# Kernel optimization log

Hardware: AMD Instinct MI355X
Metric: run time of the kernel (lower is better)

## Reference

```python
import jax, jax.numpy as jnp
import numpy as np

EPS = 1e-5

def _ln(t, g, b):
    m = t.mean(-1, keepdims=True)
    v = ((t - m) ** 2).mean(-1, keepdims=True)
    return (t - m) * jax.lax.rsqrt(v + EPS) * g + b

def _sr(t, w, b, H, W, sr):
    # t: [B, H*W, C] -> spatial-reduction conv -> [B, (H//sr)*(W//sr), C]
    B, L, C = t.shape
    xi = t.transpose(0, 2, 1).reshape(B, C, H, W)
    y = jax.lax.conv_general_dilated(xi, w, (sr, sr), 'VALID',
                                     dimension_numbers=('NCHW', 'OIHW', 'NCHW'))
    return y.reshape(B, C, -1).transpose(0, 2, 1) + b

def setup_inputs() -> dict:
    key = jax.random.key(0)
    ks = jax.random.split(key, 9)
    C, head, sr, H, W = 128, 2, 2, 64, 64
    B, N = 4, 2 * H * W
    s = 0.02
    return {
        'x': jax.random.normal(ks[0], (B, N, C), jnp.float32),
        'qW': jax.random.normal(ks[1], (C, C), jnp.float32) * s,
        'qb': jnp.zeros((C,), jnp.float32),
        'kvW': jax.random.normal(ks[2], (C, 2 * C), jnp.float32) * s,
        'kvb': jnp.zeros((2 * C,), jnp.float32),
        'projW': jax.random.normal(ks[3], (C, C), jnp.float32) * s,
        'projb': jnp.zeros((C,), jnp.float32),
        'srW': jax.random.normal(ks[4], (C, C, sr, sr), jnp.float32) * s,
        'srb': jnp.zeros((C,), jnp.float32),
        'lnW': jnp.ones((C,), jnp.float32),
        'lnB': jnp.zeros((C,), jnp.float32),
        'H': H, 'W': W, 'fuse': 1,
    }

def reference(x, qW, qb, kvW, kvb, projW, projb, srW, srb, lnW, lnB, H, W, fuse):
    head, sr = 2, 2
    B, N, C = x.shape
    Dh = C // head
    scale = Dh ** -0.5
    q = (x @ qW + qb).reshape(B, N, head, Dh).transpose(0, 2, 1, 3)  # [B,h,N,Dh]
    mask = None
    if fuse and sr > 1:
        half = N // 2
        x_rgb = _ln(_sr(x[:, :half, :], srW, srb, H, W, sr), lnW, lnB)
        x_dte = _ln(_sr(x[:, half:, :], srW, srb, H, W, sr), lnW, lnB)
        xkv = jnp.concatenate([x_rgb, x_dte], axis=1)
        M = N // (sr * sr)
        row = jnp.arange(N)[:, None] < half            # query in rgb half
        col = jnp.arange(M)[None, :] < (M // 2)        # key in rgb half
        mask = row == col                              # True on same-modality blocks -> masked
    elif sr > 1:
        xkv = _ln(_sr(x, srW, srb, H, W, sr), lnW, lnB)
    else:
        xkv = x
    M = xkv.shape[1]
    kv = (xkv @ kvW + kvb).reshape(B, M, 2, head, Dh).transpose(2, 0, 3, 1, 4)
    k, v = kv[0], kv[1]                                # [B,h,M,Dh]
    attn = jnp.einsum('bhnd,bhmd->bhnm', q, k) * scale
    if mask is not None:
        attn = jnp.where(mask[None, None], -jnp.inf, attn)
    attn = jax.nn.softmax(attn, axis=-1)
    out = jnp.einsum('bhnm,bhmd->bhnd', attn, v).transpose(0, 2, 1, 3).reshape(B, N, C)
    return out @ projW + projb
```

## Files before the change

### kernel.cpp

```cpp
#include <hip/hip_runtime.h>
#include <hip/hip_bf16.h>

#define LN_EPS 1e-5f

typedef __attribute__((ext_vector_type(8))) short bf16x8_t;
typedef __attribute__((ext_vector_type(4))) float f32x4_t;
typedef __attribute__((ext_vector_type(4))) unsigned short u16x4_t;

#define MFMA16(a, b, c) __builtin_amdgcn_mfma_f32_16x16x32_bf16(a, b, c, 0, 0, 0)

__device__ inline unsigned short f2bf(float f) {
    union { float f; unsigned int u; } v; v.f = f;
    unsigned int r = v.u + 0x7fffu + ((v.u >> 16) & 1u);
    return (unsigned short)(r >> 16);
}

__device__ inline u16x4_t pk4(float a, float b, float c, float d) {
    union { u16x4_t v; __hip_bfloat162 h[2]; } u;
    u.h[0] = __float22bfloat162_rn(float2{a, b});
    u.h[1] = __float22bfloat162_rn(float2{c, d});
    return u.v;
}

__device__ inline size_t fragidx(int row, int k, int KC) {
    return ((size_t)((row >> 4) * KC + (k >> 5))) * 512 +
           (((k >> 3) & 3) * 16 + (row & 15)) * 8 + (k & 7);
}

__global__ void k_prep_w(const float* __restrict__ qW, const float* __restrict__ kvW,
                         const float* __restrict__ projW, const float* __restrict__ srW,
                         unsigned short* __restrict__ qWs, unsigned short* __restrict__ kvWs,
                         unsigned short* __restrict__ projWs, unsigned short* __restrict__ srWs) {
    int i = blockIdx.x * 256 + threadIdx.x;
    if (i < 16384) {
        int n = i & 127, k = i >> 7;
        qWs[fragidx(n, k, 4)] = f2bf(qW[k * 128 + n]);
    } else if (i < 49152) {
        int j = i - 16384; int n = j & 255, k = j >> 8;
        kvWs[fragidx(n, k, 4)] = f2bf(kvW[k * 256 + n]);
    } else if (i < 65536) {
        int j = i - 49152; int n = j & 127, k = j >> 7;
        projWs[fragidx(n, k, 4)] = f2bf(projW[k * 128 + n]);
    } else {
        int j = i - 65536; int n = j >> 9, rem = j & 511, q = rem >> 7, c = rem & 127;
        srWs[fragidx(n, q * 128 + c, 16)] = f2bf(srW[n * 512 + c * 4 + q]);
    }
}

__global__ void k_prep_x(const float* __restrict__ x, unsigned short* __restrict__ xsw,
                         unsigned short* __restrict__ Psw) {
    int i = blockIdx.x * 256 + threadIdx.x;
    int c4 = i & 31;
    int row = i >> 5;
    float4 v = *(const float4*)(x + (size_t)row * 128 + c4 * 4);
    u16x4_t o = pk4(v.x, v.y, v.z, v.w);
    int ch = c4 * 4;
    *(u16x4_t*)(xsw + fragidx(row, ch, 4)) = o;
    int b = row >> 13, n = row & 8191;
    int hf = n >> 12, rem = n & 4095;
    int y = rem >> 6, xc = rem & 63;
    int oy = y >> 1, ky = y & 1, ox = xc >> 1, kx = xc & 1;
    int q = ky * 2 + kx;
    int pos = b * 2048 + hf * 1024 + oy * 32 + ox;
    *(u16x4_t*)(Psw + fragidx(pos, q * 128 + ch, 16)) = o;
}

__global__ __launch_bounds__(256)
void k_convkv(const unsigned short* __restrict__ Psw, const unsigned short* __restrict__ srWs,
              const float* __restrict__ srb, const float* __restrict__ lnW,
              const float* __restrict__ lnB, const unsigned short* __restrict__ kvWs,
              const float* __restrict__ kvb, unsigned short* __restrict__ ksw,
              unsigned short* __restrict__ vsw) {
    const int t = threadIdx.x, w = t >> 6, lane = t & 63;
    const int col = lane & 15, quad = lane >> 4;
    const int rt_l = w >> 1, hf = w & 1;
    const int RT = blockIdx.x * 2 + rt_l;

    __shared__ unsigned short xkvs[2 * 4 * 512];
    __shared__ float lnred[4][16][2];

    f32x4_t acc[4] = {};
    {
        const unsigned short* xp = Psw + (size_t)RT * 16 * 512 + lane * 8;
        const unsigned short* wp = srWs + (size_t)hf * 4 * 16 * 512 + lane * 8;
        for (int kc = 0; kc < 16; kc++) {
            bf16x8_t xb = *(const bf16x8_t*)(xp + (size_t)kc * 512);
            #pragma unroll
            for (int j = 0; j < 4; j++) {
                bf16x8_t wf = *(const bf16x8_t*)(wp + (size_t)(j * 16 + kc) * 512);
                acc[j] = MFMA16(wf, xb, acc[j]);
            }
        }
    }
    float s = 0.f, ss = 0.f;
    #pragma unroll
    for (int j = 0; j < 4; j++) {
        float4 bs = *(const float4*)(srb + hf * 64 + j * 16 + quad * 4);
        acc[j][0] += bs.x; acc[j][1] += bs.y; acc[j][2] += bs.z; acc[j][3] += bs.w;
        #pragma unroll
        for (int r = 0; r < 4; r++) { float v = acc[j][r]; s += v; ss += v * v; }
    }
    s += __shfl_xor(s, 16, 64);  s += __shfl_xor(s, 32, 64);
    ss += __shfl_xor(ss, 16, 64); ss += __shfl_xor(ss, 32, 64);
    if (lane < 16) { lnred[w][lane][0] = s; lnred[w][lane][1] = ss; }
    __syncthreads();
    float stot = s + lnred[w ^ 1][col][0];
    float sstot = ss + lnred[w ^ 1][col][1];
    float mean = stot * (1.0f / 128.0f);
    float var = sstot * (1.0f / 128.0f) - mean * mean;
    float rs = rsqrtf(var + LN_EPS);
    #pragma unroll
    for (int j = 0; j < 4; j++) {
        int f0 = hf * 64 + j * 16 + quad * 4;
        float4 g = *(const float4*)(lnW + f0);
        float4 be = *(const float4*)(lnB + f0);
        u16x4_t o = pk4((acc[j][0] - mean) * rs * g.x + be.x,
                        (acc[j][1] - mean) * rs * g.y + be.y,
                        (acc[j][2] - mean) * rs * g.z + be.z,
                        (acc[j][3] - mean) * rs * g.w + be.w);
        *(u16x4_t*)(xkvs + ((size_t)(rt_l * 4 + (f0 >> 5))) * 512 +
                    (((f0 >> 3) & 3) * 16 + col) * 8 + (f0 & 7)) = o;
    }
    __syncthreads();
    bf16x8_t xf[2][4];
    #pragma unroll
    for (int rt = 0; rt < 2; rt++)
        #pragma unroll
        for (int kc = 0; kc < 4; kc++)
            xf[rt][kc] = *(const bf16x8_t*)(xkvs + (size_t)(rt * 4 + kc) * 512 + lane * 8);
    #pragma unroll
    for (int i = 0; i < 2; i++) {
        const int nt2 = w * 2 + i;
        f32x4_t aK[2] = {};
        #pragma unroll
        for (int kc = 0; kc < 4; kc++) {
            bf16x8_t wf = *(const bf16x8_t*)(kvWs + (size_t)(nt2 * 4 + kc) * 512 + lane * 8);
            aK[0] = MFMA16(wf, xf[0][kc], aK[0]);
            aK[1] = MFMA16(wf, xf[1][kc], aK[1]);
        }
        float4 bs = *(const float4*)(kvb + nt2 * 16 + quad * 4);
        #pragma unroll
        for (int rt = 0; rt < 2; rt++) {
            int p = (blockIdx.x * 2 + rt) * 16 + col;
            int m = p & 2047, bb = p >> 11;
            int bh = bb * 2 + (nt2 >> 2);
            u16x4_t o = pk4(aK[rt][0] + bs.x, aK[rt][1] + bs.y,
                            aK[rt][2] + bs.z, aK[rt][3] + bs.w);
            *(u16x4_t*)(ksw + ((size_t)(bh * 128 + (m >> 4)) * 2 + ((nt2 >> 1) & 1)) * 512 +
                        (((nt2 & 1) * 2 + (quad >> 1)) * 16 + (m & 15)) * 8 + (quad & 1) * 4) = o;
        }
    }
    #pragma unroll
    for (int i = 0; i < 2; i++) {
        const int nt2 = 8 + w * 2 + i;
        f32x4_t aV[2] = {};
        #pragma unroll
        for (int kc = 0; kc < 4; kc++) {
            bf16x8_t wf = *(const bf16x8_t*)(kvWs + (size_t)(nt2 * 4 + kc) * 512 + lane * 8);
            aV[0] = MFMA16(xf[0][kc], wf, aV[0]);
            aV[1] = MFMA16(xf[1][kc], wf, aV[1]);
        }
        int fv = (nt2 - 8) * 16 + col;
        int h = fv >> 6, dd = fv & 63;
        float bv = kvb[128 + fv];
        #pragma unroll
        for (int rt = 0; rt < 2; rt++) {
            int G = (blockIdx.x * 2 + rt) * 16 + quad * 4;
            int bb = G >> 11, m0 = G & 2047;
            int bh = bb * 2 + h;
            u16x4_t o = pk4(aV[rt][0] + bv, aV[rt][1] + bv,
                            aV[rt][2] + bv, aV[rt][3] + bv);
            *(u16x4_t*)(vsw + ((size_t)((bh * 4 + (dd >> 4)) * 64 + (m0 >> 5))) * 512 +
                        (((m0 >> 3) & 3) * 16 + (dd & 15)) * 8 + (m0 & 7)) = o;
        }
    }
}

__global__ __launch_bounds__(512)
void k_attn_f(const unsigned short* __restrict__ xsw, const unsigned short* __restrict__ qWs,
              const float* __restrict__ qb, const unsigned short* __restrict__ ksw,
              const unsigned short* __restrict__ vsw, const unsigned short* __restrict__ projWs,
              const float* __restrict__ projb, float* __restrict__ out) {
    const int blkx = blockIdx.x, mod = blockIdx.y, b = blockIdx.z;
    const int t = threadIdx.x, w = t >> 6, lane = t & 63;
    const int col = lane & 15, quad = lane >> 4;
    const int qt = w & 3, h = w >> 2;
    const int bh = b * 2 + h;

    __shared__ unsigned short qls[16 * 512];
    __shared__ unsigned short pp[8][16][72];

    {
        const int qtile_g = b * 512 + mod * 256 + blkx * 4 + qt;
        f32x4_t acc[4] = {};
        const unsigned short* xp = xsw + (size_t)qtile_g * 4 * 512 + lane * 8;
        const unsigned short* wp = qWs + (size_t)h * 16 * 512 + lane * 8;
        #pragma unroll
        for (int kc = 0; kc < 4; kc++) {
            bf16x8_t xb = *(const bf16x8_t*)(xp + (size_t)kc * 512);
            #pragma unroll
            for (int j = 0; j < 4; j++) {
                bf16x8_t wf = *(const bf16x8_t*)(wp + (size_t)(j * 4 + kc) * 512);
                acc[j] = MFMA16(wf, xb, acc[j]);
            }
        }
        const float sc = 0.125f * 1.44269504089f;
        #pragma unroll
        for (int j = 0; j < 4; j++) {
            float4 bs = *(const float4*)(qb + h * 64 + j * 16 + quad * 4);
            u16x4_t o = pk4((acc[j][0] + bs.x) * sc, (acc[j][1] + bs.y) * sc,
                            (acc[j][2] + bs.z) * sc, (acc[j][3] + bs.w) * sc);
            *(u16x4_t*)(qls + ((size_t)((h * 4 + qt) * 2 + (j >> 1))) * 512 +
                        (((j & 1) * 2 + (quad >> 1)) * 16 + col) * 8 + (quad & 1) * 4) = o;
        }
    }
    const bf16x8_t qf0 = *(const bf16x8_t*)(qls + (size_t)((h * 4 + qt) * 2 + 0) * 512 + lane * 8);
    const bf16x8_t qf1 = *(const bf16x8_t*)(qls + (size_t)((h * 4 + qt) * 2 + 1) * 512 + lane * 8);

    const unsigned short* kp0 = ksw + ((size_t)(bh * 128 + (1 - mod) * 64) * 2) * 512 + lane * 8;
    const unsigned short* vp0 = vsw + ((size_t)(bh * 4) * 64 + (1 - mod) * 32) * 512 + lane * 8;
    const bf16x8_t ones = { 0x3F80, 0x3F80, 0x3F80, 0x3F80,
                            0x3F80, 0x3F80, 0x3F80, 0x3F80 };
    f32x4_t O[4] = {};
    f32x4_t accl = {};

    for (int kt = 0; kt < 16; kt++) {
        bf16x8_t kf[8], vf[8];
        #pragma unroll
        for (int i = 0; i < 8; i++)
            kf[i] = *(const bf16x8_t*)(kp0 + (size_t)(kt * 8 + i) * 512);
        #pragma unroll
        for (int dt = 0; dt < 4; dt++) {
            vf[dt * 2 + 0] = *(const bf16x8_t*)(vp0 + ((size_t)dt * 64 + kt * 2 + 0) * 512);
            vf[dt * 2 + 1] = *(const bf16x8_t*)(vp0 + ((size_t)dt * 64 + kt * 2 + 1) * 512);
        }
        f32x4_t ST[4];
        #pragma unroll
        for (int nb = 0; nb < 4; nb++) {
            f32x4_t sA = {};
            sA = MFMA16(kf[nb * 2 + 0], qf0, sA);
            sA = MFMA16(kf[nb * 2 + 1], qf1, sA);
            ST[nb] = sA;
        }
        #pragma unroll
        for (int nb = 0; nb < 4; nb++) {
            u16x4_t pk = pk4(exp2f(ST[nb][0]), exp2f(ST[nb][1]),
                             exp2f(ST[nb][2]), exp2f(ST[nb][3]));
            *(u16x4_t*)(&pp[w][col][nb * 16 + quad * 4]) = pk;
        }
        bf16x8_t pb0 = *(const bf16x8_t*)(&pp[w][col][quad * 8]);
        bf16x8_t pb1 = *(const bf16x8_t*)(&pp[w][col][32 + quad * 8]);
        accl = MFMA16(ones, pb0, accl);
        accl = MFMA16(ones, pb1, accl);
        #pragma unroll
        for (int dt = 0; dt < 4; dt++) {
            O[dt] = MFMA16(vf[dt * 2 + 0], pb0, O[dt]);
            O[dt] = MFMA16(vf[dt * 2 + 1], pb1, O[dt]);
        }
    }
    __syncthreads();
    {
        float rl = 1.0f / accl[0];
        #pragma unroll
        for (int dt = 0; dt < 4; dt++) {
            u16x4_t o = pk4(O[dt][0] * rl, O[dt][1] * rl, O[dt][2] * rl, O[dt][3] * rl);
            *(u16x4_t*)(qls + ((size_t)(qt * 4 + h * 2 + (dt >> 1))) * 512 +
                        (((dt & 1) * 2 + (quad >> 1)) * 16 + col) * 8 + (quad & 1) * 4) = o;
        }
    }
    __syncthreads();
    {
        const int qt2 = w & 3, nh = w >> 2;
        f32x4_t acc[4] = {};
        const unsigned short* wp = projWs + (size_t)nh * 16 * 512 + lane * 8;
        #pragma unroll
        for (int kc = 0; kc < 4; kc++) {
            bf16x8_t ob = *(const bf16x8_t*)(qls + (size_t)(qt2 * 4 + kc) * 512 + lane * 8);
            #pragma unroll
            for (int j = 0; j < 4; j++) {
                bf16x8_t wf = *(const bf16x8_t*)(wp + (size_t)(j * 4 + kc) * 512);
                acc[j] = MFMA16(wf, ob, acc[j]);
            }
        }
        const int n = b * 8192 + mod * 4096 + blkx * 64 + qt2 * 16 + col;
        #pragma unroll
        for (int j = 0; j < 4; j++) {
            int f0 = nh * 64 + j * 16 + quad * 4;
            float4 bs = *(const float4*)(projb + f0);
            float4 o = { acc[j][0] + bs.x, acc[j][1] + bs.y,
                         acc[j][2] + bs.z, acc[j][3] + bs.w };
            *(float4*)(out + (size_t)n * 128 + f0) = o;
        }
    }
}

extern "C" void kernel_launch(void* const* d_in, const int* in_sizes, int n_in,
                              void* d_out, int out_size, void* d_ws, size_t ws_size,
                              hipStream_t stream) {
    const float* x     = (const float*)d_in[0];
    const float* qW    = (const float*)d_in[1];
    const float* qb    = (const float*)d_in[2];
    const float* kvW   = (const float*)d_in[3];
    const float* kvb   = (const float*)d_in[4];
    const float* projW = (const float*)d_in[5];
    const float* projb = (const float*)d_in[6];
    const float* srW   = (const float*)d_in[7];
    const float* srb   = (const float*)d_in[8];
    const float* lnW   = (const float*)d_in[9];
    const float* lnB   = (const float*)d_in[10];

    char* ws = (char*)d_ws;
    unsigned short* qWs    = (unsigned short*)(ws + 0);
    unsigned short* kvWs   = (unsigned short*)(ws + 32768);
    unsigned short* projWs = (unsigned short*)(ws + 98304);
    unsigned short* srWs   = (unsigned short*)(ws + 131072);
    unsigned short* xsw    = (unsigned short*)(ws + 262144);
    unsigned short* Psw    = (unsigned short*)(ws + 8650752);
    unsigned short* ksw    = (unsigned short*)(ws + 17039360);
    unsigned short* vsw    = (unsigned short*)(ws + 19136512);

    k_prep_w<<<dim3(512), dim3(256), 0, stream>>>(qW, kvW, projW, srW,
                                                  qWs, kvWs, projWs, srWs);
    k_prep_x<<<dim3(4096), dim3(256), 0, stream>>>(x, xsw, Psw);
    k_convkv<<<dim3(256), dim3(256), 0, stream>>>(Psw, srWs, srb, lnW, lnB,
                                                  kvWs, kvb, ksw, vsw);
    k_attn_f<<<dim3(64, 2, 4), dim3(512), 0, stream>>>(xsw, qWs, qb, ksw, vsw,
                                                       projWs, projb, (float*)d_out);
}
```

Baseline: 149.1 us.

## Restructure attention to reuse K/V over two query tiles, keep P in registers

```diff
diff --git a/kernel.cpp b/kernel.cpp
--- a/kernel.cpp
+++ b/kernel.cpp
@@ -4,10 +4,12 @@
 #define LN_EPS 1e-5f
 
 typedef __attribute__((ext_vector_type(8))) short bf16x8_t;
+typedef __attribute__((ext_vector_type(4))) short bf16x4_t;
 typedef __attribute__((ext_vector_type(4))) float f32x4_t;
 typedef __attribute__((ext_vector_type(4))) unsigned short u16x4_t;
 
-#define MFMA16(a, b, c) __builtin_amdgcn_mfma_f32_16x16x32_bf16(a, b, c, 0, 0, 0)
+#define MFMA32(a, b, c) __builtin_amdgcn_mfma_f32_16x16x32_bf16(a, b, c, 0, 0, 0)
+#define MFMA16(a, b, c) __builtin_amdgcn_mfma_f32_16x16x16bf16_1k(a, b, c, 0, 0, 0)
 
 __device__ inline unsigned short f2bf(float f) {
     union { float f; unsigned int u; } v; v.f = f;
@@ -19,6 +21,20 @@
     union { u16x4_t v; __hip_bfloat162 h[2]; } u;
     u.h[0] = __float22bfloat162_rn(float2{a, b});
     u.h[1] = __float22bfloat162_rn(float2{c, d});
+    return u.v;
+}
+__device__ inline bf16x4_t pk4b(float a, float b, float c, float d) {
+    union { bf16x4_t v; __hip_bfloat162 h[2]; } u;
+    u.h[0] = __float22bfloat162_rn(float2{a, b});
+    u.h[1] = __float22bfloat162_rn(float2{c, d});
+    return u.v;
+}
+__device__ inline bf16x8_t pk8(float4 a, float4 b) {
+    union { bf16x8_t v; __hip_bfloat162 h[4]; } u;
+    u.h[0] = __float22bfloat162_rn(float2{a.x, a.y});
+    u.h[1] = __float22bfloat162_rn(float2{a.z, a.w});
+    u.h[2] = __float22bfloat162_rn(float2{b.x, b.y});
+    u.h[3] = __float22bfloat162_rn(float2{b.z, b.w});
     return u.v;
 }
 
@@ -47,15 +63,13 @@
     }
 }
 
-__global__ void k_prep_x(const float* __restrict__ x, unsigned short* __restrict__ xsw,
-                         unsigned short* __restrict__ Psw) {
+__global__ void k_prep_x(const float* __restrict__ x, unsigned short* __restrict__ Psw) {
     int i = blockIdx.x * 256 + threadIdx.x;
     int c4 = i & 31;
     int row = i >> 5;
     float4 v = *(const float4*)(x + (size_t)row * 128 + c4 * 4);
     u16x4_t o = pk4(v.x, v.y, v.z, v.w);
     int ch = c4 * 4;
-    *(u16x4_t*)(xsw + fragidx(row, ch, 4)) = o;
     int b = row >> 13, n = row & 8191;
     int hf = n >> 12, rem = n & 4095;
     int y = rem >> 6, xc = rem & 63;
@@ -70,222 +84,229 @@
               const float* __restrict__ srb, const float* __restrict__ lnW,
               const float* __restrict__ lnB, const unsigned short* __restrict__ kvWs,
               const float* __restrict__ kvb, unsigned short* __restrict__ ksw,
-              unsigned short* __restrict__ vsw) {
+              unsigned short* __restrict__ vls) {
     const int t = threadIdx.x, w = t >> 6, lane = t & 63;
     const int col = lane & 15, quad = lane >> 4;
-    const int rt_l = w >> 1, hf = w & 1;
-    const int RT = blockIdx.x * 2 + rt_l;
-
-    __shared__ unsigned short xkvs[2 * 4 * 512];
+    const int RT = blockIdx.x;
+
+    __shared__ unsigned short xs[4 * 512];
     __shared__ float lnred[4][16][2];
 
-    f32x4_t acc[4] = {};
+    f32x4_t acc[2] = {};
     {
         const unsigned short* xp = Psw + (size_t)RT * 16 * 512 + lane * 8;
-        const unsigned short* wp = srWs + (size_t)hf * 4 * 16 * 512 + lane * 8;
+        const unsigned short* wp = srWs + lane * 8;
         for (int kc = 0; kc < 16; kc++) {
             bf16x8_t xb = *(const bf16x8_t*)(xp + (size_t)kc * 512);
             #pragma unroll
-            for (int j = 0; j < 4; j++) {
-                bf16x8_t wf = *(const bf16x8_t*)(wp + (size_t)(j * 16 + kc) * 512);
-                acc[j] = MFMA16(wf, xb, acc[j]);
+            for (int jj = 0; jj < 2; jj++) {
+                bf16x8_t wf = *(const bf16x8_t*)(wp + (size_t)((w * 2 + jj) * 16 + kc) * 512);
+                acc[jj] = MFMA32(wf, xb, acc[jj]);
             }
         }
     }
     float s = 0.f, ss = 0.f;
     #pragma unroll
-    for (int j = 0; j < 4; j++) {
-        float4 bs = *(const float4*)(srb + hf * 64 + j * 16 + quad * 4);
-        acc[j][0] += bs.x; acc[j][1] += bs.y; acc[j][2] += bs.z; acc[j][3] += bs.w;
-        #pragma unroll
-        for (int r = 0; r < 4; r++) { float v = acc[j][r]; s += v; ss += v * v; }
+    for (int jj = 0; jj < 2; jj++) {
+        float4 bs = *(const float4*)(srb + (w * 2 + jj) * 16 + quad * 4);
+        acc[jj][0] += bs.x; acc[jj][1] += bs.y; acc[jj][2] += bs.z; acc[jj][3] += bs.w;
+        #pragma unroll
+        for (int r = 0; r < 4; r++) { float v = acc[jj][r]; s += v; ss += v * v; }
     }
     s += __shfl_xor(s, 16, 64);  s += __shfl_xor(s, 32, 64);
     ss += __shfl_xor(ss, 16, 64); ss += __shfl_xor(ss, 32, 64);
     if (lane < 16) { lnred[w][lane][0] = s; lnred[w][lane][1] = ss; }
     __syncthreads();
-    float stot = s + lnred[w ^ 1][col][0];
-    float sstot = ss + lnred[w ^ 1][col][1];
+    float stot = 0.f, sstot = 0.f;
+    #pragma unroll
+    for (int ww = 0; ww < 4; ww++) { stot += lnred[ww][col][0]; sstot += lnred[ww][col][1]; }
     float mean = stot * (1.0f / 128.0f);
     float var = sstot * (1.0f / 128.0f) - mean * mean;
     float rs = rsqrtf(var + LN_EPS);
     #pragma unroll
-    for (int j = 0; j < 4; j++) {
-        int f0 = hf * 64 + j * 16 + quad * 4;
+    for (int jj = 0; jj < 2; jj++) {
+        int f0 = (w * 2 + jj) * 16 + quad * 4;
         float4 g = *(const float4*)(lnW + f0);
         float4 be = *(const float4*)(lnB + f0);
-        u16x4_t o = pk4((acc[j][0] - mean) * rs * g.x + be.x,
-                        (acc[j][1] - mean) * rs * g.y + be.y,
-                        (acc[j][2] - mean) * rs * g.z + be.z,
-                        (acc[j][3] - mean) * rs * g.w + be.w);
-        *(u16x4_t*)(xkvs + ((size_t)(rt_l * 4 + (f0 >> 5))) * 512 +
+        u16x4_t o = pk4((acc[jj][0] - mean) * rs * g.x + be.x,
+                        (acc[jj][1] - mean) * rs * g.y + be.y,
+                        (acc[jj][2] - mean) * rs * g.z + be.z,
+                        (acc[jj][3] - mean) * rs * g.w + be.w);
+        *(u16x4_t*)(xs + ((size_t)(f0 >> 5)) * 512 +
                     (((f0 >> 3) & 3) * 16 + col) * 8 + (f0 & 7)) = o;
     }
     __syncthreads();
-    bf16x8_t xf[2][4];
-    #pragma unroll
-    for (int rt = 0; rt < 2; rt++)
-        #pragma unroll
-        for (int kc = 0; kc < 4; kc++)
-            xf[rt][kc] = *(const bf16x8_t*)(xkvs + (size_t)(rt * 4 + kc) * 512 + lane * 8);
-    #pragma unroll
-    for (int i = 0; i < 2; i++) {
-        const int nt2 = w * 2 + i;
-        f32x4_t aK[2] = {};
+    bf16x8_t xf[4];
+    #pragma unroll
+    for (int kc = 0; kc < 4; kc++)
+        xf[kc] = *(const bf16x8_t*)(xs + (size_t)kc * 512 + lane * 8);
+    const int p0 = RT * 16;
+    const int bb = p0 >> 11;
+    #pragma unroll
+    for (int jj = 0; jj < 2; jj++) {
+        const int nt = w * 2 + jj;
+        f32x4_t aK = {};
         #pragma unroll
         for (int kc = 0; kc < 4; kc++) {
-            bf16x8_t wf = *(const bf16x8_t*)(kvWs + (size_t)(nt2 * 4 + kc) * 512 + lane * 8);
-            aK[0] = MFMA16(wf, xf[0][kc], aK[0]);
-            aK[1] = MFMA16(wf, xf[1][kc], aK[1]);
-        }
-        float4 bs = *(const float4*)(kvb + nt2 * 16 + quad * 4);
-        #pragma unroll
-        for (int rt = 0; rt < 2; rt++) {
-            int p = (blockIdx.x * 2 + rt) * 16 + col;
-            int m = p & 2047, bb = p >> 11;
-            int bh = bb * 2 + (nt2 >> 2);
-            u16x4_t o = pk4(aK[rt][0] + bs.x, aK[rt][1] + bs.y,
-                            aK[rt][2] + bs.z, aK[rt][3] + bs.w);
-            *(u16x4_t*)(ksw + ((size_t)(bh * 128 + (m >> 4)) * 2 + ((nt2 >> 1) & 1)) * 512 +
-                        (((nt2 & 1) * 2 + (quad >> 1)) * 16 + (m & 15)) * 8 + (quad & 1) * 4) = o;
-        }
-    }
-    #pragma unroll
-    for (int i = 0; i < 2; i++) {
-        const int nt2 = 8 + w * 2 + i;
-        f32x4_t aV[2] = {};
+            bf16x8_t wf = *(const bf16x8_t*)(kvWs + (size_t)(nt * 4 + kc) * 512 + lane * 8);
+            aK = MFMA32(wf, xf[kc], aK);
+        }
+        float4 bs = *(const float4*)(kvb + nt * 16 + quad * 4);
+        int m = (p0 + col) & 2047;
+        int bh = bb * 2 + (nt >> 2);
+        int d0 = (nt & 3) * 16 + quad * 4;
+        u16x4_t o = pk4(aK[0] + bs.x, aK[1] + bs.y, aK[2] + bs.z, aK[3] + bs.w);
+        *(u16x4_t*)(ksw + ((size_t)(bh * 128 + (m >> 4)) * 2 + (d0 >> 5)) * 512 +
+                    (((d0 >> 3) & 3) * 16 + (m & 15)) * 8 + (d0 & 7)) = o;
+    }
+    #pragma unroll
+    for (int jj = 0; jj < 2; jj++) {
+        const int nt = w * 2 + jj;
+        f32x4_t aV = {};
         #pragma unroll
         for (int kc = 0; kc < 4; kc++) {
-            bf16x8_t wf = *(const bf16x8_t*)(kvWs + (size_t)(nt2 * 4 + kc) * 512 + lane * 8);
-            aV[0] = MFMA16(xf[0][kc], wf, aV[0]);
-            aV[1] = MFMA16(xf[1][kc], wf, aV[1]);
-        }
-        int fv = (nt2 - 8) * 16 + col;
+            bf16x8_t wf = *(const bf16x8_t*)(kvWs + (size_t)((8 + nt) * 4 + kc) * 512 + lane * 8);
+            aV = MFMA32(xf[kc], wf, aV);
+        }
+        int fv = nt * 16 + col;
         int h = fv >> 6, dd = fv & 63;
         float bv = kvb[128 + fv];
-        #pragma unroll
-        for (int rt = 0; rt < 2; rt++) {
-            int G = (blockIdx.x * 2 + rt) * 16 + quad * 4;
-            int bb = G >> 11, m0 = G & 2047;
-            int bh = bb * 2 + h;
-            u16x4_t o = pk4(aV[rt][0] + bv, aV[rt][1] + bv,
-                            aV[rt][2] + bv, aV[rt][3] + bv);
-            *(u16x4_t*)(vsw + ((size_t)((bh * 4 + (dd >> 4)) * 64 + (m0 >> 5))) * 512 +
-                        (((m0 >> 3) & 3) * 16 + (dd & 15)) * 8 + (m0 & 7)) = o;
-        }
-    }
-}
-
-__global__ __launch_bounds__(512)
-void k_attn_f(const unsigned short* __restrict__ xsw, const unsigned short* __restrict__ qWs,
-              const float* __restrict__ qb, const unsigned short* __restrict__ ksw,
-              const unsigned short* __restrict__ vsw, const unsigned short* __restrict__ projWs,
-              const float* __restrict__ projb, float* __restrict__ out) {
+        int m0 = (p0 + quad * 4) & 2047;
+        int bh = bb * 2 + h;
+        int kt = m0 >> 6, nb = (m0 >> 4) & 3;
+        u16x4_t o = pk4(aV[0] + bv, aV[1] + bv, aV[2] + bv, aV[3] + bv);
+        *(u16x4_t*)(vls + (((size_t)(bh * 32 + kt) * 4 + (dd >> 4)) * 2 + (nb >> 1)) * 512 +
+                    (quad * 16 + (dd & 15)) * 8 + (nb & 1) * 4) = o;
+    }
+}
+
+__global__ __launch_bounds__(256)
+void k_attn_f2(const float* __restrict__ x, const unsigned short* __restrict__ qWs,
+               const float* __restrict__ qb, const unsigned short* __restrict__ ksw,
+               const unsigned short* __restrict__ vls, const unsigned short* __restrict__ projWs,
+               const float* __restrict__ projb, float* __restrict__ out) {
     const int blkx = blockIdx.x, mod = blockIdx.y, b = blockIdx.z;
     const int t = threadIdx.x, w = t >> 6, lane = t & 63;
     const int col = lane & 15, quad = lane >> 4;
-    const int qt = w & 3, h = w >> 2;
+    const int qg = w & 1, h = w >> 1;
     const int bh = b * 2 + h;
-
-    __shared__ unsigned short qls[16 * 512];
-    __shared__ unsigned short pp[8][16][72];
-
-    {
-        const int qtile_g = b * 512 + mod * 256 + blkx * 4 + qt;
+    const int qbase = mod * 4096 + blkx * 64 + qg * 32;
+
+    __shared__ unsigned short sbuf[64 * 136];
+
+    unsigned short* qarea = sbuf + w * 2048;
+    const float sc = 0.125f * 1.44269504089f;
+    #pragma unroll
+    for (int qt = 0; qt < 2; qt++) {
+        const float* xrow = x + ((size_t)b * 8192 + qbase + qt * 16 + col) * 128;
         f32x4_t acc[4] = {};
-        const unsigned short* xp = xsw + (size_t)qtile_g * 4 * 512 + lane * 8;
-        const unsigned short* wp = qWs + (size_t)h * 16 * 512 + lane * 8;
         #pragma unroll
         for (int kc = 0; kc < 4; kc++) {
-            bf16x8_t xb = *(const bf16x8_t*)(xp + (size_t)kc * 512);
+            float4 xa = *(const float4*)(xrow + kc * 32 + quad * 8);
+            float4 xb2 = *(const float4*)(xrow + kc * 32 + quad * 8 + 4);
+            bf16x8_t xf = pk8(xa, xb2);
             #pragma unroll
             for (int j = 0; j < 4; j++) {
-                bf16x8_t wf = *(const bf16x8_t*)(wp + (size_t)(j * 4 + kc) * 512);
-                acc[j] = MFMA16(wf, xb, acc[j]);
-            }
-        }
-        const float sc = 0.125f * 1.44269504089f;
+                bf16x8_t wf = *(const bf16x8_t*)(qWs + (size_t)((h * 4 + j) * 4 + kc) * 512 + lane * 8);
+                acc[j] = MFMA32(wf, xf, acc[j]);
+            }
+        }
         #pragma unroll
         for (int j = 0; j < 4; j++) {
             float4 bs = *(const float4*)(qb + h * 64 + j * 16 + quad * 4);
             u16x4_t o = pk4((acc[j][0] + bs.x) * sc, (acc[j][1] + bs.y) * sc,
                             (acc[j][2] + bs.z) * sc, (acc[j][3] + bs.w) * sc);
-            *(u16x4_t*)(qls + ((size_t)((h * 4 + qt) * 2 + (j >> 1))) * 512 +
+            *(u16x4_t*)(qarea + ((size_t)(qt * 2 + (j >> 1))) * 512 +
                         (((j & 1) * 2 + (quad >> 1)) * 16 + col) * 8 + (quad & 1) * 4) = o;
         }
     }
-    const bf16x8_t qf0 = *(const bf16x8_t*)(qls + (size_t)((h * 4 + qt) * 2 + 0) * 512 + lane * 8);
-    const bf16x8_t qf1 = *(const bf16x8_t*)(qls + (size_t)((h * 4 + qt) * 2 + 1) * 512 + lane * 8);
-
-    const unsigned short* kp0 = ksw + ((size_t)(bh * 128 + (1 - mod) * 64) * 2) * 512 + lane * 8;
-    const unsigned short* vp0 = vsw + ((size_t)(bh * 4) * 64 + (1 - mod) * 32) * 512 + lane * 8;
-    const bf16x8_t ones = { 0x3F80, 0x3F80, 0x3F80, 0x3F80,
-                            0x3F80, 0x3F80, 0x3F80, 0x3F80 };
-    f32x4_t O[4] = {};
-    f32x4_t accl = {};
+    bf16x8_t qf[2][2];
+    #pragma unroll
+    for (int qt = 0; qt < 2; qt++)
+        #pragma unroll
+        for (int kc = 0; kc < 2; kc++)
+            qf[qt][kc] = *(const bf16x8_t*)(qarea + (size_t)(qt * 2 + kc) * 512 + lane * 8);
+    __syncthreads();
+
+    const unsigned short* kp0 =
+        ksw + ((size_t)(bh * 128 + (1 - mod) * 64) * 2) * 512 + lane * 8;
+    const unsigned short* vp0 =
+        vls + ((size_t)(bh * 32 + (1 - mod) * 16) * 8) * 512 + lane * 8;
+    const bf16x4_t ones4 = { 0x3F80, 0x3F80, 0x3F80, 0x3F80 };
+
+    f32x4_t O[2][4] = {};
+    f32x4_t accl[2] = {};
 
     for (int kt = 0; kt < 16; kt++) {
-        bf16x8_t kf[8], vf[8];
+        bf16x8_t kf[8];
         #pragma unroll
         for (int i = 0; i < 8; i++)
             kf[i] = *(const bf16x8_t*)(kp0 + (size_t)(kt * 8 + i) * 512);
-        #pragma unroll
-        for (int dt = 0; dt < 4; dt++) {
-            vf[dt * 2 + 0] = *(const bf16x8_t*)(vp0 + ((size_t)dt * 64 + kt * 2 + 0) * 512);
-            vf[dt * 2 + 1] = *(const bf16x8_t*)(vp0 + ((size_t)dt * 64 + kt * 2 + 1) * 512);
-        }
-        f32x4_t ST[4];
-        #pragma unroll
-        for (int nb = 0; nb < 4; nb++) {
-            f32x4_t sA = {};
-            sA = MFMA16(kf[nb * 2 + 0], qf0, sA);
-            sA = MFMA16(kf[nb * 2 + 1], qf1, sA);
-            ST[nb] = sA;
-        }
-        #pragma unroll
-        for (int nb = 0; nb < 4; nb++) {
-            u16x4_t pk = pk4(exp2f(ST[nb][0]), exp2f(ST[nb][1]),
-                             exp2f(ST[nb][2]), exp2f(ST[nb][3]));
-            *(u16x4_t*)(&pp[w][col][nb * 16 + quad * 4]) = pk;
-        }
-        bf16x8_t pb0 = *(const bf16x8_t*)(&pp[w][col][quad * 8]);
-        bf16x8_t pb1 = *(const bf16x8_t*)(&pp[w][col][32 + quad * 8]);
-        accl = MFMA16(ones, pb0, accl);
-        accl = MFMA16(ones, pb1, accl);
-        #pragma unroll
-        for (int dt = 0; dt < 4; dt++) {
-            O[dt] = MFMA16(vf[dt * 2 + 0], pb0, O[dt]);
-            O[dt] = MFMA16(vf[dt * 2 + 1], pb1, O[dt]);
+        union { bf16x8_t v8; bf16x4_t v4[2]; } vf[8];
+        #pragma unroll
+        for (int i = 0; i < 8; i++)
+            vf[i].v8 = *(const bf16x8_t*)(vp0 + (size_t)(kt * 8 + i) * 512);
+        f32x4_t ST[2][4];
+        #pragma unroll
+        for (int qt = 0; qt < 2; qt++)
+            #pragma unroll
+            for (int nb = 0; nb < 4; nb++) {
+                f32x4_t sA = {};
+                sA = MFMA32(kf[nb * 2 + 0], qf[qt][0], sA);
+                sA = MFMA32(kf[nb * 2 + 1], qf[qt][1], sA);
+                ST[qt][nb] = sA;
+            }
+        bf16x4_t pa[2][4];
+        #pragma unroll
+        for (int qt = 0; qt < 2; qt++)
+            #pragma unroll
+            for (int nb = 0; nb < 4; nb++)
+                pa[qt][nb] = pk4b(exp2f(ST[qt][nb][0]), exp2f(ST[qt][nb][1]),
+                                  exp2f(ST[qt][nb][2]), exp2f(ST[qt][nb][3]));
+        #pragma unroll
+        for (int qt = 0; qt < 2; qt++) {
+            #pragma unroll
+            for (int nb = 0; nb < 4; nb++) {
+                accl[qt] = MFMA16(pa[qt][nb], ones4, accl[qt]);
+                #pragma unroll
+                for (int dt = 0; dt < 4; dt++)
+                    O[qt][dt] = MFMA16(pa[qt][nb], vf[dt * 2 + (nb >> 1)].v4[nb & 1], O[qt][dt]);
+            }
+        }
+    }
+
+    #pragma unroll
+    for (int qt = 0; qt < 2; qt++) {
+        #pragma unroll
+        for (int r = 0; r < 4; r++) {
+            float rl = 1.0f / accl[qt][r];
+            int qrow = qg * 32 + qt * 16 + quad * 4 + r;
+            #pragma unroll
+            for (int dt = 0; dt < 4; dt++)
+                sbuf[qrow * 136 + h * 64 + dt * 16 + col] = f2bf(O[qt][dt][r] * rl);
         }
     }
     __syncthreads();
     {
-        float rl = 1.0f / accl[0];
-        #pragma unroll
-        for (int dt = 0; dt < 4; dt++) {
-            u16x4_t o = pk4(O[dt][0] * rl, O[dt][1] * rl, O[dt][2] * rl, O[dt][3] * rl);
-            *(u16x4_t*)(qls + ((size_t)(qt * 4 + h * 2 + (dt >> 1))) * 512 +
-                        (((dt & 1) * 2 + (quad >> 1)) * 16 + col) * 8 + (quad & 1) * 4) = o;
-        }
-    }
-    __syncthreads();
-    {
-        const int qt2 = w & 3, nh = w >> 2;
-        f32x4_t acc[4] = {};
-        const unsigned short* wp = projWs + (size_t)nh * 16 * 512 + lane * 8;
-        #pragma unroll
-        for (int kc = 0; kc < 4; kc++) {
-            bf16x8_t ob = *(const bf16x8_t*)(qls + (size_t)(qt2 * 4 + kc) * 512 + lane * 8);
-            #pragma unroll
-            for (int j = 0; j < 4; j++) {
-                bf16x8_t wf = *(const bf16x8_t*)(wp + (size_t)(j * 4 + kc) * 512);
-                acc[j] = MFMA16(wf, ob, acc[j]);
-            }
-        }
+        const int qt2 = w;
+        bf16x8_t ob[4];
+        #pragma unroll
+        for (int kc = 0; kc < 4; kc++)
+            ob[kc] = *(const bf16x8_t*)(sbuf + (size_t)(qt2 * 16 + col) * 136 + kc * 32 + quad * 8);
+        f32x4_t acc[8];
+        #pragma unroll
+        for (int j = 0; j < 8; j++) acc[j] = f32x4_t{};
+        #pragma unroll
+        for (int kc = 0; kc < 4; kc++)
+            #pragma unroll
+            for (int j = 0; j < 8; j++) {
+                bf16x8_t wf = *(const bf16x8_t*)(projWs + (size_t)(j * 4 + kc) * 512 + lane * 8);
+                acc[j] = MFMA32(wf, ob[kc], acc[j]);
+            }
         const int n = b * 8192 + mod * 4096 + blkx * 64 + qt2 * 16 + col;
         #pragma unroll
-        for (int j = 0; j < 4; j++) {
-            int f0 = nh * 64 + j * 16 + quad * 4;
+        for (int j = 0; j < 8; j++) {
+            int f0 = j * 16 + quad * 4;
             float4 bs = *(const float4*)(projb + f0);
             float4 o = { acc[j][0] + bs.x, acc[j][1] + bs.y,
                          acc[j][2] + bs.z, acc[j][3] + bs.w };
@@ -314,16 +335,15 @@
     unsigned short* kvWs   = (unsigned short*)(ws + 32768);
     unsigned short* projWs = (unsigned short*)(ws + 98304);
     unsigned short* srWs   = (unsigned short*)(ws + 131072);
-    unsigned short* xsw    = (unsigned short*)(ws + 262144);
-    unsigned short* Psw    = (unsigned short*)(ws + 8650752);
-    unsigned short* ksw    = (unsigned short*)(ws + 17039360);
-    unsigned short* vsw    = (unsigned short*)(ws + 19136512);
+    unsigned short* Psw    = (unsigned short*)(ws + 262144);
+    unsigned short* ksw    = (unsigned short*)(ws + 8650752);
+    unsigned short* vls    = (unsigned short*)(ws + 10747904);
 
     k_prep_w<<<dim3(512), dim3(256), 0, stream>>>(qW, kvW, projW, srW,
                                                   qWs, kvWs, projWs, srWs);
-    k_prep_x<<<dim3(4096), dim3(256), 0, stream>>>(x, xsw, Psw);
-    k_convkv<<<dim3(256), dim3(256), 0, stream>>>(Psw, srWs, srb, lnW, lnB,
-                                                  kvWs, kvb, ksw, vsw);
-    k_attn_f<<<dim3(64, 2, 4), dim3(512), 0, stream>>>(xsw, qWs, qb, ksw, vsw,
-                                                       projWs, projb, (float*)d_out);
-}
+    k_prep_x<<<dim3(4096), dim3(256), 0, stream>>>(x, Psw);
+    k_convkv<<<dim3(512), dim3(256), 0, stream>>>(Psw, srWs, srb, lnW, lnB,
+                                                  kvWs, kvb, ksw, vls);
+    k_attn_f2<<<dim3(64, 2, 4), dim3(256), 0, stream>>>(x, qWs, qb, ksw, vls,
+                                                        projWs, projb, (float*)d_out);
+}
```

Result: no change. 146.8 us (-1.5%).
